# Kernel optimization log

Hardware: AMD Instinct MI355X
Metric: run time of the kernel (lower is better)

The kernel has to match this reference:

```python
import jax, jax.numpy as jnp
import numpy as np

EMB = 1024
HEADS = 16
HEAD_DIM = EMB // HEADS
CTX = 2048
BATCH = 4
LN_EPS = 1e-5


def layer_norm(x, g, b):
    mu = jnp.mean(x, axis=-1, keepdims=True)
    var = jnp.mean(jnp.square(x - mu), axis=-1, keepdims=True)
    return (x - mu) * jax.lax.rsqrt(var + LN_EPS) * g + b


def setup_inputs() -> dict:
    key = jax.random.key(0)
    ks = jax.random.split(key, 12)
    s_in = 1.0 / np.sqrt(EMB)
    s_ff = 1.0 / np.sqrt(4 * EMB)
    return {
        "x": jax.random.normal(ks[0], (BATCH, CTX, EMB), jnp.float32),
        # per-head Q/K/V projections, no bias (matches Head linears)
        "wq": jax.random.normal(ks[1], (HEADS, EMB, HEAD_DIM), jnp.float32) * s_in,
        "wk": jax.random.normal(ks[2], (HEADS, EMB, HEAD_DIM), jnp.float32) * s_in,
        "wv": jax.random.normal(ks[3], (HEADS, EMB, HEAD_DIM), jnp.float32) * s_in,
        "w_proj": jax.random.normal(ks[4], (EMB, EMB), jnp.float32) * s_in,
        "b_proj": jnp.zeros((EMB,), jnp.float32),
        "w1": jax.random.normal(ks[5], (EMB, 4 * EMB), jnp.float32) * s_in,
        "b1": jnp.zeros((4 * EMB,), jnp.float32),
        "w2": jax.random.normal(ks[6], (4 * EMB, EMB), jnp.float32) * s_ff,
        "b2": jnp.zeros((EMB,), jnp.float32),
        "ln1_g": jnp.ones((EMB,), jnp.float32),
        "ln1_b": jnp.zeros((EMB,), jnp.float32),
        "ln2_g": jnp.ones((EMB,), jnp.float32),
        "ln2_b": jnp.zeros((EMB,), jnp.float32),
    }


def reference(x, wq, wk, wv, w_proj, b_proj, w1, b1, w2, b2, ln1_g, ln1_b, ln2_g, ln2_b):
    B, T, C = x.shape
    # --- attention branch (pre-LN) ---
    h = layer_norm(x, ln1_g, ln1_b)
    q = jnp.einsum('btc,hcd->bhtd', h, wq)
    k = jnp.einsum('btc,hcd->bhtd', h, wk)
    v = jnp.einsum('btc,hcd->bhtd', h, wv)
    scale = 1.0 / np.sqrt(HEAD_DIM)
    scores = jnp.einsum('bhtd,bhsd->bhts', q, k) * scale  # [B,H,T,T]
    causal = jnp.tril(jnp.ones((T, T), dtype=bool))
    scores = jnp.where(causal, scores, -jnp.inf)
    attn = jax.nn.softmax(scores, axis=-1)
    out = jnp.einsum('bhts,bhsd->bhtd', attn, v)
    out = out.transpose(0, 2, 1, 3).reshape(B, T, C)  # concat heads
    out = out @ w_proj.T + b_proj if False else jnp.einsum('btc,cd->btd', out, w_proj) + b_proj
    x = x + out
    # --- FFN branch (pre-LN) ---
    h2 = layer_norm(x, ln2_g, ln2_b)
    ff = jax.nn.relu(jnp.einsum('btc,cf->btf', h2, w1) + b1)
    ff = jnp.einsum('btf,fc->btc', ff, w2) + b2
    return x + ff
```

## Files before the change

kernel.cpp:

```cpp
#include <hip/hip_runtime.h>


#define DEVI __device__ __forceinline__

typedef float  f32x4  __attribute__((ext_vector_type(4)));
typedef __bf16 bf16x8 __attribute__((ext_vector_type(8)));
typedef short  s16x8  __attribute__((ext_vector_type(8)));
typedef unsigned short u16;

DEVI u16 f2bf(float f) {
    return __builtin_bit_cast(u16, (__bf16)f);
}

DEVI void gload_lds16(const void* g, void* l) {
    __builtin_amdgcn_global_load_lds(
        (__attribute__((address_space(1))) void*)(g),
        (__attribute__((address_space(3))) void*)(l), 16, 0, 0);
}

DEVI f32x4 mfma16(s16x8 a, s16x8 b, f32x4 c) {
    return __builtin_amdgcn_mfma_f32_16x16x32_bf16(
        __builtin_bit_cast(bf16x8, a), __builtin_bit_cast(bf16x8, b), c, 0, 0, 0);
}

__global__ __launch_bounds__(256) void transpose_cvt(
    const float* __restrict__ src, u16* __restrict__ dst,
    int K, int N, long srcStride, long dstStride)
{
    __shared__ float t[64][65];
    src += (long)blockIdx.z * srcStride;
    dst += (long)blockIdx.z * dstStride;
    int k0 = blockIdx.x * 64, n0 = blockIdx.y * 64;
    int tx = threadIdx.x & 63, ty = threadIdx.x >> 6;
#pragma unroll
    for (int i = 0; i < 16; ++i) {
        int r = ty * 16 + i;
        t[r][tx] = src[(long)(k0 + r) * N + n0 + tx];
    }
    __syncthreads();
#pragma unroll
    for (int i = 0; i < 16; ++i) {
        int r = ty * 16 + i;
        dst[(long)(n0 + r) * K + k0 + tx] = f2bf(t[tx][r]);
    }
}

__global__ __launch_bounds__(256) void ln_bf16(
    const float* __restrict__ x, const float* __restrict__ g,
    const float* __restrict__ b, u16* __restrict__ out)
{
    int row = blockIdx.x, tid = threadIdx.x;
    const float4 v = ((const float4*)(x + (long)row * 1024))[tid];
    float s = v.x + v.y + v.z + v.w;
    float q = v.x * v.x + v.y * v.y + v.z * v.z + v.w * v.w;
#pragma unroll
    for (int m = 1; m < 64; m <<= 1) { s += __shfl_xor(s, m); q += __shfl_xor(q, m); }
    __shared__ float red[8];
    int lane = tid & 63, w = tid >> 6;
    if (lane == 0) { red[w] = s; red[w + 4] = q; }
    __syncthreads();
    s = red[0] + red[1] + red[2] + red[3];
    q = red[4] + red[5] + red[6] + red[7];
    float mu  = s * (1.0f / 1024.0f);
    float var = q * (1.0f / 1024.0f) - mu * mu;
    float rs  = rsqrtf(var + 1e-5f);
    float4 gv = ((const float4*)g)[tid];
    float4 bv = ((const float4*)b)[tid];
    ushort4 o;
    o.x = f2bf((v.x - mu) * rs * gv.x + bv.x);
    o.y = f2bf((v.y - mu) * rs * gv.y + bv.y);
    o.z = f2bf((v.z - mu) * rs * gv.z + bv.z);
    o.w = f2bf((v.w - mu) * rs * gv.w + bv.w);
    ((ushort4*)(out + (long)row * 1024))[tid] = o;
}

template <int EPI>
__global__ __launch_bounds__(256, 3) void gemm_bt(
    const u16* __restrict__ A, const u16* __restrict__ Bt,
    int M, int N, int K,
    float* __restrict__ outF, u16* __restrict__ outB,
    const float* __restrict__ bias, const float* __restrict__ resid,
    u16* __restrict__ qd, u16* __restrict__ kd, u16* __restrict__ vd)
{
    __shared__ alignas(16) u16 As[128 * 32];
    __shared__ alignas(16) u16 Bs[128 * 32];
    int tid = threadIdx.x;
    int lane = tid & 63, w = tid >> 6;
    int wm = w & 1, wn = w >> 1;
    int l15 = lane & 15, l4 = lane >> 4;
    long m0 = (long)blockIdx.x * 128, n0 = (long)blockIdx.y * 128;
    const u16* Ag = A + m0 * K;
    const u16* Bg = Bt + n0 * K;
    int scol = (lane & 3) * 8;
    int srow0 = (w * 2 + 0) * 16 + (lane >> 2);
    int srow1 = (w * 2 + 1) * 16 + (lane >> 2);

    f32x4 acc[4][4] = {};

    for (int kt = 0; kt < K; kt += 32) {
        gload_lds16(Ag + (long)srow0 * K + kt + scol, &As[(w * 2 + 0) * 512]);
        gload_lds16(Ag + (long)srow1 * K + kt + scol, &As[(w * 2 + 1) * 512]);
        gload_lds16(Bg + (long)srow0 * K + kt + scol, &Bs[(w * 2 + 0) * 512]);
        gload_lds16(Bg + (long)srow1 * K + kt + scol, &Bs[(w * 2 + 1) * 512]);
        __syncthreads();
        s16x8 a[4], b[4];
#pragma unroll
        for (int m = 0; m < 4; ++m)
            a[m] = *(const s16x8*)&As[(wm * 64 + m * 16 + l15) * 32 + l4 * 8];
#pragma unroll
        for (int n = 0; n < 4; ++n)
            b[n] = *(const s16x8*)&Bs[(wn * 64 + n * 16 + l15) * 32 + l4 * 8];
#pragma unroll
        for (int m = 0; m < 4; ++m)
#pragma unroll
            for (int n = 0; n < 4; ++n)
                acc[m][n] = mfma16(a[m], b[n], acc[m][n]);
        __syncthreads();
    }

    long mbase = m0 + wm * 64;
    long nbase = n0 + wn * 64;
#pragma unroll
    for (int m = 0; m < 4; ++m)
#pragma unroll
        for (int n = 0; n < 4; ++n)
#pragma unroll
            for (int r = 0; r < 4; ++r) {
                long row = mbase + m * 16 + l4 * 4 + r;
                long col = nbase + n * 16 + l15;
                float val = acc[m][n][r];
                if constexpr (EPI == 0) {
                    int c = (int)col;
                    int which = c >> 10, hh = (c >> 6) & 15, dd = c & 63;
                    int bb = (int)(row >> 11), tt = (int)(row & 2047);
                    if (which == 2) {
                        vd[((long)(bb * 16 + hh) * 64 + dd) * 2048 + tt] = f2bf(val);
                    } else {
                        u16* dst = which == 0 ? qd : kd;
                        dst[((long)(bb * 16 + hh) * 2048 + tt) * 64 + dd] = f2bf(val);
                    }
                } else if constexpr (EPI == 1) {
                    outF[row * N + col] = val + bias[col] + resid[row * N + col];
                } else {
                    float t2 = val + bias[col];
                    outB[row * N + col] = f2bf(t2 > 0.f ? t2 : 0.f);
                }
            }
}

__global__ __launch_bounds__(256, 2) void attn_kernel(
    const u16* __restrict__ Q, const u16* __restrict__ K,
    const u16* __restrict__ Vt, u16* __restrict__ O)
{
    constexpr int PAD = 72;
    constexpr float SC2 = 0.125f * 1.44269504088896f;
    constexpr float THR = 11.5416f;
    __shared__ alignas(16) u16 Ks[2][64 * PAD];
    __shared__ alignas(16) u16 Vts[2][64 * PAD];
    __shared__ alignas(16) u16 Ps[4 * 32 * PAD];
    int tid = threadIdx.x, lane = tid & 63, w = tid >> 6;
    int l15 = lane & 15, l4 = lane >> 4;
    int qp = blockIdx.x, hh = blockIdx.y, bb = blockIdx.z;
    const long hbase = ((long)(bb * 16 + hh)) * 2048 * 64;
    u16* pw = &Ps[w * 32 * PAD];
    int rdswz = (l15 >> 2) & 3;

    int srow[2], scol8[2];
#pragma unroll
    for (int i = 0; i < 2; ++i) {
        int c = tid + 256 * i;
        srow[i] = c >> 3;
        scol8[i] = (c & 7) * 8;
    }

#pragma unroll 1
    for (int ph = 0; ph < 2; ++ph) {
        int qt = ph == 0 ? qp : 15 - qp;
        int q0w = qt * 128 + w * 32;
        int nt = 2 * qt + 2;

        s16x8 aq[2][2];
#pragma unroll
        for (int m = 0; m < 2; ++m)
#pragma unroll
            for (int kk = 0; kk < 2; ++kk)
                aq[m][kk] = *(const s16x8*)&Q[hbase + (long)(q0w + m * 16 + l15) * 64 + kk * 32 + l4 * 8];

        f32x4 o[2][4] = {};
        float mrow[2][4], lrow[2][4];
#pragma unroll
        for (int m = 0; m < 2; ++m)
#pragma unroll
            for (int r = 0; r < 4; ++r) { mrow[m][r] = -1e30f; lrow[m][r] = 0.f; }

        s16x8 kr[2], vr[2];
        {
            const u16* Kg = K + hbase;
            const u16* Vg = Vt + hbase;
#pragma unroll
            for (int i = 0; i < 2; ++i) {
                s16x8 k0 = *(const s16x8*)&Kg[srow[i] * 64 + scol8[i]];
                s16x8 v0 = *(const s16x8*)&Vg[(long)srow[i] * 2048 + scol8[i]];
                *(s16x8*)&Ks[0][srow[i] * PAD + scol8[i]]  = k0;
                *(s16x8*)&Vts[0][srow[i] * PAD + scol8[i]] = v0;
            }
            if (nt > 1) {
                const u16* Kg1 = K + hbase + 64 * 64;
                const u16* Vg1 = Vt + hbase + 64;
#pragma unroll
                for (int i = 0; i < 2; ++i) {
                    kr[i] = *(const s16x8*)&Kg1[srow[i] * 64 + scol8[i]];
                    vr[i] = *(const s16x8*)&Vg1[(long)srow[i] * 2048 + scol8[i]];
                }
            }
        }
        __syncthreads();

#pragma unroll 1
        for (int kt = 0; kt < nt; ++kt) {
            int cur = kt & 1;
            if (kt + 1 < nt) {
#pragma unroll
                for (int i = 0; i < 2; ++i) {
                    *(s16x8*)&Ks[cur ^ 1][srow[i] * PAD + scol8[i]]  = kr[i];
                    *(s16x8*)&Vts[cur ^ 1][srow[i] * PAD + scol8[i]] = vr[i];
                }
            }
            if (kt + 2 < nt) {
                const u16* Kg = K + hbase + (long)(kt + 2) * 64 * 64;
                const u16* Vg = Vt + hbase + (long)(kt + 2) * 64;
#pragma unroll
                for (int i = 0; i < 2; ++i) {
                    kr[i] = *(const s16x8*)&Kg[srow[i] * 64 + scol8[i]];
                    vr[i] = *(const s16x8*)&Vg[(long)srow[i] * 2048 + scol8[i]];
                }
            }

            s16x8 bk[4][2];
#pragma unroll
            for (int n = 0; n < 4; ++n)
#pragma unroll
                for (int kk = 0; kk < 2; ++kk)
                    bk[n][kk] = *(const s16x8*)&Ks[cur][(n * 16 + l15) * PAD + kk * 32 + l4 * 8];

            bool needMask = (kt * 64 + 63 > q0w);
#pragma unroll
            for (int m = 0; m < 2; ++m) {
                f32x4 s[4];
                __builtin_amdgcn_s_setprio(1);
#pragma unroll
                for (int n = 0; n < 4; ++n) {
                    f32x4 z = {0.f, 0.f, 0.f, 0.f};
                    z = mfma16(aq[m][0], bk[n][0], z);
                    z = mfma16(aq[m][1], bk[n][1], z);
                    s[n] = z;
                }
                __builtin_amdgcn_s_setprio(0);
                float pm[4] = {-1e30f, -1e30f, -1e30f, -1e30f};
#pragma unroll
                for (int n = 0; n < 4; ++n)
#pragma unroll
                    for (int r = 0; r < 4; ++r) {
                        float sv = s[n][r] * SC2;
                        if (needMask) {
                            int kglob = kt * 64 + n * 16 + l15;
                            int qglob = q0w + m * 16 + l4 * 4 + r;
                            if (kglob > qglob) sv = -1e30f;
                        }
                        s[n][r] = sv;
                        pm[r] = fmaxf(pm[r], sv);
                    }
#pragma unroll
                for (int xm = 1; xm < 16; xm <<= 1)
#pragma unroll
                    for (int r = 0; r < 4; ++r) pm[r] = fmaxf(pm[r], __shfl_xor(pm[r], xm));

                bool okl = true;
#pragma unroll
                for (int r = 0; r < 4; ++r) okl = okl && (pm[r] - mrow[m][r] <= THR);
                int allok = __all(okl);
                float ef[4];
                if (!allok) {
#pragma unroll
                    for (int r = 0; r < 4; ++r) {
                        float mn = fmaxf(mrow[m][r], pm[r]);
                        ef[r] = exp2f(mrow[m][r] - mn);
                        mrow[m][r] = mn;
                    }
                }
                float rsum[4] = {0.f, 0.f, 0.f, 0.f};
#pragma unroll
                for (int n = 0; n < 4; ++n)
#pragma unroll
                    for (int r = 0; r < 4; ++r) {
                        float p = exp2f(s[n][r] - mrow[m][r]);
                        s[n][r] = p;
                        rsum[r] += p;
                    }
#pragma unroll
                for (int xm = 1; xm < 16; xm <<= 1)
#pragma unroll
                    for (int r = 0; r < 4; ++r) rsum[r] += __shfl_xor(rsum[r], xm);
                if (!allok) {
#pragma unroll
                    for (int r = 0; r < 4; ++r) lrow[m][r] = lrow[m][r] * ef[r] + rsum[r];
#pragma unroll
                    for (int n = 0; n < 4; ++n)
#pragma unroll
                        for (int r = 0; r < 4; ++r) o[m][n][r] *= ef[r];
                } else {
#pragma unroll
                    for (int r = 0; r < 4; ++r) lrow[m][r] += rsum[r];
                }

#pragma unroll
                for (int n = 0; n < 4; ++n) {
                    int chunkp = ((n * 2 + (l15 >> 3)) ^ l4) * 8 + (l15 & 7);
#pragma unroll
                    for (int r = 0; r < 4; ++r)
                        pw[(m * 16 + l4 * 4 + r) * PAD + chunkp] = f2bf(s[n][r]);
                }
            }

            s16x8 pa[2][2], bv[4][2];
#pragma unroll
            for (int m = 0; m < 2; ++m)
#pragma unroll
                for (int kk = 0; kk < 2; ++kk)
                    pa[m][kk] = *(const s16x8*)&pw[(m * 16 + l15) * PAD + (kk * 4 + (l4 ^ rdswz)) * 8];
#pragma unroll
            for (int n = 0; n < 4; ++n)
#pragma unroll
                for (int kk = 0; kk < 2; ++kk)
                    bv[n][kk] = *(const s16x8*)&Vts[cur][(n * 16 + l15) * PAD + kk * 32 + l4 * 8];
            __builtin_amdgcn_s_setprio(1);
#pragma unroll
            for (int m = 0; m < 2; ++m)
#pragma unroll
                for (int n = 0; n < 4; ++n) {
                    o[m][n] = mfma16(pa[m][0], bv[n][0], o[m][n]);
                    o[m][n] = mfma16(pa[m][1], bv[n][1], o[m][n]);
                }
            __builtin_amdgcn_s_setprio(0);
            __syncthreads();
        }

#pragma unroll
        for (int m = 0; m < 2; ++m) {
            float invl[4];
#pragma unroll
            for (int r = 0; r < 4; ++r) invl[r] = 1.0f / lrow[m][r];
#pragma unroll
            for (int n = 0; n < 4; ++n)
#pragma unroll
                for (int r = 0; r < 4; ++r) {
                    int t = q0w + m * 16 + l4 * 4 + r;
                    O[((long)(bb * 2048 + t)) * 1024 + hh * 64 + n * 16 + l15] =
                        f2bf(o[m][n][r] * invl[r]);
                }
        }
        __syncthreads();
    }
}

extern "C" void kernel_launch(void* const* d_in, const int* in_sizes, int n_in,
                              void* d_out, int out_size, void* d_ws, size_t ws_size,
                              hipStream_t stream)
{
    const float* x      = (const float*)d_in[0];
    const float* wq     = (const float*)d_in[1];
    const float* wk     = (const float*)d_in[2];
    const float* wv     = (const float*)d_in[3];
    const float* w_proj = (const float*)d_in[4];
    const float* b_proj = (const float*)d_in[5];
    const float* w1     = (const float*)d_in[6];
    const float* b1     = (const float*)d_in[7];
    const float* w2     = (const float*)d_in[8];
    const float* b2     = (const float*)d_in[9];
    const float* ln1_g  = (const float*)d_in[10];
    const float* ln1_b  = (const float*)d_in[11];
    const float* ln2_g  = (const float*)d_in[12];
    const float* ln2_b  = (const float*)d_in[13];

    char* ws = (char*)d_ws;
    u16*   WQKVt = (u16*)(ws + 0);
    u16*   WPt   = (u16*)(ws + 6291456);
    u16*   W1t   = (u16*)(ws + 8388608);
    u16*   W2t   = (u16*)(ws + 16777216);
    u16*   H     = (u16*)(ws + 25165824);
    u16*   Qb    = (u16*)(ws + 41943040);
    u16*   Kb    = (u16*)(ws + 58720256);
    u16*   Vb    = (u16*)(ws + 75497472);
    u16*   Ob    = (u16*)(ws + 92274688);
    u16*   FF    = (u16*)(ws + 41943040);
    float* X1    = (float*)(ws + 109051904);
    float* out   = (float*)d_out;

    transpose_cvt<<<dim3(16, 1, 16), 256, 0, stream>>>(wq, WQKVt,           1024, 64, 65536, 65536);
    transpose_cvt<<<dim3(16, 1, 16), 256, 0, stream>>>(wk, WQKVt + 1048576, 1024, 64, 65536, 65536);
    transpose_cvt<<<dim3(16, 1, 16), 256, 0, stream>>>(wv, WQKVt + 2097152, 1024, 64, 65536, 65536);
    transpose_cvt<<<dim3(16, 16, 1), 256, 0, stream>>>(w_proj, WPt, 1024, 1024, 0, 0);
    transpose_cvt<<<dim3(16, 64, 1), 256, 0, stream>>>(w1, W1t, 1024, 4096, 0, 0);
    transpose_cvt<<<dim3(64, 16, 1), 256, 0, stream>>>(w2, W2t, 4096, 1024, 0, 0);

    ln_bf16<<<8192, 256, 0, stream>>>(x, ln1_g, ln1_b, H);

    gemm_bt<0><<<dim3(64, 24), 256, 0, stream>>>(H, WQKVt, 8192, 3072, 1024,
        nullptr, nullptr, nullptr, nullptr, Qb, Kb, Vb);

    attn_kernel<<<dim3(8, 16, 4), 256, 0, stream>>>(Qb, Kb, Vb, Ob);

    gemm_bt<1><<<dim3(64, 8), 256, 0, stream>>>(Ob, WPt, 8192, 1024, 1024,
        X1, nullptr, b_proj, x, nullptr, nullptr, nullptr);

    ln_bf16<<<8192, 256, 0, stream>>>(X1, ln2_g, ln2_b, H);

    gemm_bt<2><<<dim3(64, 32), 256, 0, stream>>>(H, W1t, 8192, 4096, 1024,
        nullptr, FF, b1, nullptr, nullptr, nullptr, nullptr);

    gemm_bt<1><<<dim3(64, 8), 256, 0, stream>>>(FF, W2t, 8192, 1024, 4096,
        out, nullptr, b2, X1, nullptr, nullptr, nullptr);
}
```

Baseline: 463.5 us.

## Rewrite attention with 32x32 MFMA, transposed S and register-resident P

```diff
diff --git a/kernel.cpp b/kernel.cpp
--- a/kernel.cpp
+++ b/kernel.cpp
@@ -4,12 +4,18 @@
 #define DEVI __device__ __forceinline__
 
 typedef float  f32x4  __attribute__((ext_vector_type(4)));
+typedef float  f32x16 __attribute__((ext_vector_type(16)));
 typedef __bf16 bf16x8 __attribute__((ext_vector_type(8)));
 typedef short  s16x8  __attribute__((ext_vector_type(8)));
+typedef unsigned int u32x4 __attribute__((ext_vector_type(4)));
 typedef unsigned short u16;
 
 DEVI u16 f2bf(float f) {
     return __builtin_bit_cast(u16, (__bf16)f);
+}
+
+DEVI unsigned pk2(float lo, float hi2) {
+    return (unsigned)f2bf(lo) | ((unsigned)f2bf(hi2) << 16);
 }
 
 DEVI void gload_lds16(const void* g, void* l) {
@@ -20,6 +26,11 @@
 
 DEVI f32x4 mfma16(s16x8 a, s16x8 b, f32x4 c) {
     return __builtin_amdgcn_mfma_f32_16x16x32_bf16(
+        __builtin_bit_cast(bf16x8, a), __builtin_bit_cast(bf16x8, b), c, 0, 0, 0);
+}
+
+DEVI f32x16 mfma32(s16x8 a, s16x8 b, f32x16 c) {
+    return __builtin_amdgcn_mfma_f32_32x32x16_bf16(
         __builtin_bit_cast(bf16x8, a), __builtin_bit_cast(bf16x8, b), c, 0, 0, 0);
 }
 
@@ -148,7 +159,7 @@
             }
 }
 
-__global__ __launch_bounds__(256, 2) void attn_kernel(
+__global__ __launch_bounds__(256, 4) void attn_kernel(
     const u16* __restrict__ Q, const u16* __restrict__ K,
     const u16* __restrict__ Vt, u16* __restrict__ O)
 {
@@ -157,13 +168,12 @@
     constexpr float THR = 11.5416f;
     __shared__ alignas(16) u16 Ks[2][64 * PAD];
     __shared__ alignas(16) u16 Vts[2][64 * PAD];
-    __shared__ alignas(16) u16 Ps[4 * 32 * PAD];
+    __shared__ alignas(16) float xbuf[4][32];
     int tid = threadIdx.x, lane = tid & 63, w = tid >> 6;
-    int l15 = lane & 15, l4 = lane >> 4;
+    int l31 = lane & 31, hi = lane >> 5;
+    bool h = (hi != 0);
     int qp = blockIdx.x, hh = blockIdx.y, bb = blockIdx.z;
     const long hbase = ((long)(bb * 16 + hh)) * 2048 * 64;
-    u16* pw = &Ps[w * 32 * PAD];
-    int rdswz = (l15 >> 2) & 3;
 
     int srow[2], scol8[2];
 #pragma unroll
@@ -178,20 +188,15 @@
         int qt = ph == 0 ? qp : 15 - qp;
         int q0w = qt * 128 + w * 32;
         int nt = 2 * qt + 2;
-
-        s16x8 aq[2][2];
-#pragma unroll
-        for (int m = 0; m < 2; ++m)
-#pragma unroll
-            for (int kk = 0; kk < 2; ++kk)
-                aq[m][kk] = *(const s16x8*)&Q[hbase + (long)(q0w + m * 16 + l15) * 64 + kk * 32 + l4 * 8];
-
-        f32x4 o[2][4] = {};
-        float mrow[2][4], lrow[2][4];
-#pragma unroll
-        for (int m = 0; m < 2; ++m)
-#pragma unroll
-            for (int r = 0; r < 4; ++r) { mrow[m][r] = -1e30f; lrow[m][r] = 0.f; }
+        int qv = q0w + l31;
+
+        s16x8 bq[4];
+#pragma unroll
+        for (int c = 0; c < 4; ++c)
+            bq[c] = *(const s16x8*)&Q[hbase + (long)(q0w + l31) * 64 + c * 16 + hi * 8];
+
+        f32x16 o0 = {}, o1 = {};
+        float mrow = -1e30f, lrow = 0.f;
 
         s16x8 kr[2], vr[2];
         {
@@ -236,128 +241,115 @@
                 }
             }
 
-            s16x8 bk[4][2];
-#pragma unroll
-            for (int n = 0; n < 4; ++n)
-#pragma unroll
-                for (int kk = 0; kk < 2; ++kk)
-                    bk[n][kk] = *(const s16x8*)&Ks[cur][(n * 16 + l15) * PAD + kk * 32 + l4 * 8];
-
-            bool needMask = (kt * 64 + 63 > q0w);
-#pragma unroll
-            for (int m = 0; m < 2; ++m) {
-                f32x4 s[4];
-                __builtin_amdgcn_s_setprio(1);
-#pragma unroll
-                for (int n = 0; n < 4; ++n) {
-                    f32x4 z = {0.f, 0.f, 0.f, 0.f};
-                    z = mfma16(aq[m][0], bk[n][0], z);
-                    z = mfma16(aq[m][1], bk[n][1], z);
-                    s[n] = z;
+#pragma unroll
+            for (int k2 = 0; k2 < 2; ++k2) {
+                int kbase = kt * 64 + k2 * 32;
+                if (kbase <= q0w + 31) {
+                    f32x16 s = {};
+                    __builtin_amdgcn_s_setprio(1);
+#pragma unroll
+                    for (int c = 0; c < 4; ++c) {
+                        s16x8 ak = *(const s16x8*)&Ks[cur][(k2 * 32 + l31) * PAD + c * 16 + hi * 8];
+                        s = mfma32(ak, bq[c], s);
+                    }
+                    __builtin_amdgcn_s_setprio(0);
+
+                    int khi = kbase + 4 * hi;
+                    if (kbase + 31 > q0w) {
+#pragma unroll
+                        for (int r = 0; r < 16; ++r) {
+                            int kg = khi + ((r & 3) + 8 * (r >> 2));
+                            float sv = s[r] * SC2;
+                            s[r] = (kg > qv) ? -1e30f : sv;
+                        }
+                    } else {
+#pragma unroll
+                        for (int r = 0; r < 16; ++r) s[r] *= SC2;
+                    }
+
+                    float t8[8], t4[4], t2[2];
+#pragma unroll
+                    for (int r = 0; r < 8; ++r) t8[r] = fmaxf(s[r], s[r + 8]);
+#pragma unroll
+                    for (int r = 0; r < 4; ++r) t4[r] = fmaxf(t8[r], t8[r + 4]);
+                    t2[0] = fmaxf(t4[0], t4[2]); t2[1] = fmaxf(t4[1], t4[3]);
+                    float pm = fmaxf(t2[0], t2[1]);
+                    pm = fmaxf(pm, __shfl_xor(pm, 32));
+
+                    int allok = __all(pm - mrow <= THR);
+                    float ef = 1.f;
+                    if (!allok) {
+                        float mn = fmaxf(mrow, pm);
+                        ef = exp2f(mrow - mn);
+                        mrow = mn;
+                    }
+                    float a8[8], a4[4];
+#pragma unroll
+                    for (int r = 0; r < 16; ++r) s[r] = exp2f(s[r] - mrow);
+#pragma unroll
+                    for (int r = 0; r < 8; ++r) a8[r] = s[r] + s[r + 8];
+#pragma unroll
+                    for (int r = 0; r < 4; ++r) a4[r] = a8[r] + a8[r + 4];
+                    float rsum = (a4[0] + a4[1]) + (a4[2] + a4[3]);
+                    rsum += __shfl_xor(rsum, 32);
+
+                    if (!allok) {
+                        lrow = lrow * ef + rsum;
+                        xbuf[w][l31] = ef;
+#pragma unroll
+                        for (int rr = 0; rr < 4; ++rr) {
+                            f32x4 efv = *(const f32x4*)&xbuf[w][rr * 8 + hi * 4];
+#pragma unroll
+                            for (int j = 0; j < 4; ++j) {
+                                o0[rr * 4 + j] *= efv[j];
+                                o1[rr * 4 + j] *= efv[j];
+                            }
+                        }
+                    } else {
+                        lrow += rsum;
+                    }
+
+                    unsigned c0 = pk2(s[0],  s[1]),  c1 = pk2(s[2],  s[3]);
+                    unsigned c2 = pk2(s[4],  s[5]),  c3 = pk2(s[6],  s[7]);
+                    unsigned c4 = pk2(s[8],  s[9]),  c5 = pk2(s[10], s[11]);
+                    unsigned c6 = pk2(s[12], s[13]), c7 = pk2(s[14], s[15]);
+                    unsigned x0 = __shfl_xor((int)c0, 32), x1 = __shfl_xor((int)c1, 32);
+                    unsigned x2 = __shfl_xor((int)c2, 32), x3 = __shfl_xor((int)c3, 32);
+                    unsigned x4 = __shfl_xor((int)c4, 32), x5 = __shfl_xor((int)c5, 32);
+                    unsigned x6 = __shfl_xor((int)c6, 32), x7 = __shfl_xor((int)c7, 32);
+                    u32x4 w0 = { h ? x2 : c0, h ? x3 : c1, h ? c2 : x0, h ? c3 : x1 };
+                    u32x4 w1 = { h ? x6 : c4, h ? x7 : c5, h ? c6 : x4, h ? c7 : x5 };
+                    s16x8 pa0 = __builtin_bit_cast(s16x8, w0);
+                    s16x8 pa1 = __builtin_bit_cast(s16x8, w1);
+
+                    __builtin_amdgcn_s_setprio(1);
+#pragma unroll
+                    for (int ks = 0; ks < 2; ++ks) {
+                        s16x8 pa = ks ? pa1 : pa0;
+                        s16x8 bv0 = *(const s16x8*)&Vts[cur][(l31) * PAD + k2 * 32 + ks * 16 + hi * 8];
+                        s16x8 bv1 = *(const s16x8*)&Vts[cur][(32 + l31) * PAD + k2 * 32 + ks * 16 + hi * 8];
+                        o0 = mfma32(pa, bv0, o0);
+                        o1 = mfma32(pa, bv1, o1);
+                    }
+                    __builtin_amdgcn_s_setprio(0);
                 }
-                __builtin_amdgcn_s_setprio(0);
-                float pm[4] = {-1e30f, -1e30f, -1e30f, -1e30f};
-#pragma unroll
-                for (int n = 0; n < 4; ++n)
-#pragma unroll
-                    for (int r = 0; r < 4; ++r) {
-                        float sv = s[n][r] * SC2;
-                        if (needMask) {
-                            int kglob = kt * 64 + n * 16 + l15;
-                            int qglob = q0w + m * 16 + l4 * 4 + r;
-                            if (kglob > qglob) sv = -1e30f;
-                        }
-                        s[n][r] = sv;
-                        pm[r] = fmaxf(pm[r], sv);
-                    }
-#pragma unroll
-                for (int xm = 1; xm < 16; xm <<= 1)
-#pragma unroll
-                    for (int r = 0; r < 4; ++r) pm[r] = fmaxf(pm[r], __shfl_xor(pm[r], xm));
-
-                bool okl = true;
-#pragma unroll
-                for (int r = 0; r < 4; ++r) okl = okl && (pm[r] - mrow[m][r] <= THR);
-                int allok = __all(okl);
-                float ef[4];
-                if (!allok) {
-#pragma unroll
-                    for (int r = 0; r < 4; ++r) {
-                        float mn = fmaxf(mrow[m][r], pm[r]);
-                        ef[r] = exp2f(mrow[m][r] - mn);
-                        mrow[m][r] = mn;
-                    }
-                }
-                float rsum[4] = {0.f, 0.f, 0.f, 0.f};
-#pragma unroll
-                for (int n = 0; n < 4; ++n)
-#pragma unroll
-                    for (int r = 0; r < 4; ++r) {
-                        float p = exp2f(s[n][r] - mrow[m][r]);
-                        s[n][r] = p;
-                        rsum[r] += p;
-                    }
-#pragma unroll
-                for (int xm = 1; xm < 16; xm <<= 1)
-#pragma unroll
-                    for (int r = 0; r < 4; ++r) rsum[r] += __shfl_xor(rsum[r], xm);
-                if (!allok) {
-#pragma unroll
-                    for (int r = 0; r < 4; ++r) lrow[m][r] = lrow[m][r] * ef[r] + rsum[r];
-#pragma unroll
-                    for (int n = 0; n < 4; ++n)
-#pragma unroll
-                        for (int r = 0; r < 4; ++r) o[m][n][r] *= ef[r];
-                } else {
-#pragma unroll
-                    for (int r = 0; r < 4; ++r) lrow[m][r] += rsum[r];
-                }
-
-#pragma unroll
-                for (int n = 0; n < 4; ++n) {
-                    int chunkp = ((n * 2 + (l15 >> 3)) ^ l4) * 8 + (l15 & 7);
-#pragma unroll
-                    for (int r = 0; r < 4; ++r)
-                        pw[(m * 16 + l4 * 4 + r) * PAD + chunkp] = f2bf(s[n][r]);
-                }
-            }
-
-            s16x8 pa[2][2], bv[4][2];
-#pragma unroll
-            for (int m = 0; m < 2; ++m)
-#pragma unroll
-                for (int kk = 0; kk < 2; ++kk)
-                    pa[m][kk] = *(const s16x8*)&pw[(m * 16 + l15) * PAD + (kk * 4 + (l4 ^ rdswz)) * 8];
-#pragma unroll
-            for (int n = 0; n < 4; ++n)
-#pragma unroll
-                for (int kk = 0; kk < 2; ++kk)
-                    bv[n][kk] = *(const s16x8*)&Vts[cur][(n * 16 + l15) * PAD + kk * 32 + l4 * 8];
-            __builtin_amdgcn_s_setprio(1);
-#pragma unroll
-            for (int m = 0; m < 2; ++m)
-#pragma unroll
-                for (int n = 0; n < 4; ++n) {
-                    o[m][n] = mfma16(pa[m][0], bv[n][0], o[m][n]);
-                    o[m][n] = mfma16(pa[m][1], bv[n][1], o[m][n]);
-                }
-            __builtin_amdgcn_s_setprio(0);
+            }
             __syncthreads();
         }
 
-#pragma unroll
-        for (int m = 0; m < 2; ++m) {
-            float invl[4];
-#pragma unroll
-            for (int r = 0; r < 4; ++r) invl[r] = 1.0f / lrow[m][r];
-#pragma unroll
-            for (int n = 0; n < 4; ++n)
-#pragma unroll
-                for (int r = 0; r < 4; ++r) {
-                    int t = q0w + m * 16 + l4 * 4 + r;
-                    O[((long)(bb * 2048 + t)) * 1024 + hh * 64 + n * 16 + l15] =
-                        f2bf(o[m][n][r] * invl[r]);
-                }
+        float il = 1.0f / lrow;
+        xbuf[w][l31] = il;
+        f32x4 ilv[4];
+#pragma unroll
+        for (int rr = 0; rr < 4; ++rr)
+            ilv[rr] = *(const f32x4*)&xbuf[w][rr * 8 + hi * 4];
+#pragma unroll
+        for (int r = 0; r < 16; ++r) {
+            int t = q0w + ((r & 3) + 8 * (r >> 2)) + 4 * hi;
+            float sc = ilv[r >> 2][r & 3];
+            long rbase = ((long)(bb * 2048 + t)) * 1024 + hh * 64;
+            O[rbase + l31]      = f2bf(o0[r] * sc);
+            O[rbase + 32 + l31] = f2bf(o1[r] * sc);
         }
         __syncthreads();
     }
```

Result: faster. 427.7 us (-7.7%).
